# Kernel optimization log

Hardware: AMD Instinct MI355X
Metric: run time of the kernel (lower is better)

Reference implementation:

```python
import jax, jax.numpy as jnp
import numpy as np

B, L = 4096, 200
USER_COUNT, ITEM_COUNT, CATE_COUNT = 100000, 100000, 1000
USER_DIM, ITEM_DIM, CATE_DIM = 128, 64, 64
BN_EPS = 1e-5


def setup_inputs() -> dict:
    key = jax.random.key(0)
    ks = jax.random.split(key, 16)
    # ragged history: valid prefix of `length` items (ids >= 1), zero-padded tail
    length = jax.random.randint(ks[3], (B,), 1, L + 1)
    hist_raw = jax.random.randint(ks[2], (B, L), 1, ITEM_COUNT)
    history = jnp.where(jnp.arange(L)[None, :] < length[:, None], hist_raw, 0)
    inp = {
        "user": jax.random.randint(ks[0], (B,), 0, USER_COUNT),
        "item": jax.random.randint(ks[1], (B,), 0, ITEM_COUNT),
        "history": history,
        "length": length,
        "cate_list": jax.random.randint(ks[4], (ITEM_COUNT,), 0, CATE_COUNT),
        "user_emb_W": jax.random.normal(ks[5], (USER_COUNT, USER_DIM), jnp.float32) * 0.05,
        "item_emb_W": jax.random.normal(ks[6], (ITEM_COUNT, ITEM_DIM), jnp.float32) * 0.05,
        "cate_emb_W": jax.random.normal(ks[7], (CATE_COUNT, CATE_DIM), jnp.float32) * 0.05,
        "bn_gamma": 1.0 + 0.1 * jax.random.normal(ks[8], (384,), jnp.float32),
        "bn_beta": 0.1 * jax.random.normal(ks[9], (384,), jnp.float32),
        "W1": jax.random.normal(ks[10], (200, 384), jnp.float32) * (1.0 / np.sqrt(384)),
        "b1": jnp.zeros((200,), jnp.float32),
        "a1": jnp.full((), 0.25, jnp.float32),
        "W2": jax.random.normal(ks[11], (80, 200), jnp.float32) * (1.0 / np.sqrt(200)),
        "b2": jnp.zeros((80,), jnp.float32),
        "a2": jnp.full((), 0.25, jnp.float32),
        "W3": jax.random.normal(ks[12], (2, 80), jnp.float32) * (1.0 / np.sqrt(80)),
        "b3": jnp.zeros((2,), jnp.float32),
    }
    return inp


def _prelu(x, a):
    return jnp.where(x >= 0, x, a * x)


def reference(user, item, history, length, cate_list,
              user_emb_W, item_emb_W, cate_emb_W, bn_gamma, bn_beta,
              W1, b1, a1, W2, b2, a2, W3, b3):
    u = user_emb_W[user]                                              # [B,128]
    it = jnp.concatenate([item_emb_W[item], cate_emb_W[cate_list[item]]], -1)  # [B,128]

    # Faithful replication of get_emb's loop semantics:
    # row b uses the prefix of `history[b]` up to (and incl.) the position
    # just before the first zero; a row whose first entry is 0 halts the
    # outer loop, zeroing that row and all following rows.
    nz = history != 0                                                 # [B,L]
    prefix = jnp.concatenate(
        [jnp.ones((history.shape[0], 1), bool),
         jnp.cumprod(nz[:, 1:].astype(jnp.int32), axis=1).astype(bool)], axis=1)
    row_active = jnp.cumprod(nz[:, 0].astype(jnp.int32)).astype(bool)  # outer break
    mask = prefix & row_active[:, None]                               # [B,L]

    he = jnp.concatenate([item_emb_W[history], cate_emb_W[cate_list[history]]], -1)  # [B,L,128]
    cnt = jnp.maximum(mask.sum(-1), 1).astype(he.dtype)               # [B]
    pooled = (he * mask[..., None].astype(he.dtype)).sum(1) / cnt[:, None]  # [B,128]

    x = jnp.concatenate([u, it, pooled], -1)                          # [B,384]
    # BatchNorm1d in training mode (batch stats, biased variance)
    mean = x.mean(0)
    var = x.var(0)
    x = (x - mean) * jax.lax.rsqrt(var + BN_EPS) * bn_gamma + bn_beta
    x = _prelu(x @ W1.T + b1, a1)
    x = _prelu(x @ W2.T + b2, a2)
    x = x @ W3.T + b3
    return jax.nn.softmax(x, axis=1)
```

## Files before the change

kernel.cpp:

```cpp
#include <hip/hip_runtime.h>
#include <hip/hip_bf16.h>

#define B_SZ 4096
#define L_SZ 200
#define ITEM_ELEMS 6400000
#define CATE_ELEMS 64000

typedef __bf16 bf16x8 __attribute__((ext_vector_type(8)));
typedef float  f32x4  __attribute__((ext_vector_type(4)));

static __device__ inline unsigned short bfbits(float f) {
    return __builtin_bit_cast(unsigned short, (__bf16)f);
}
static __device__ inline float bf2f(unsigned short u) {
    return __builtin_bit_cast(float, (unsigned int)u << 16);
}

__global__ __launch_bounds__(256) void k_prep(
    const float* __restrict__ W1, const float* __restrict__ W2,
    ushort* __restrict__ W1f, ushort* __restrict__ W2f,
    const int* __restrict__ history, int* __restrict__ first_bad,
    float* __restrict__ acc,
    const float* __restrict__ item_W, const float* __restrict__ cate_W,
    ushort* __restrict__ item_bf, ushort* __restrict__ cate_bf)
{
    const int bid = blockIdx.x, tid = threadIdx.x;

    if (bid < 48) {
        const int lane = tid & 63, wv = tid >> 6;
        const int t = bid * 4 + wv;
        if (t >= 191) return;
        const int nr = lane & 15, quad = lane >> 4;
        ushort v[8];
        if (t < 156) {
            const int oT = t / 12, kS = t - oT * 12;
            const int o = oT * 16 + nr;
            #pragma unroll
            for (int j = 0; j < 8; ++j) {
                int k = kS * 32 + quad * 8 + j;
                v[j] = (o < 200) ? bfbits(W1[(size_t)o * 384 + k]) : (ushort)0;
            }
            ushort* dst = W1f + ((size_t)t * 64 + lane) * 8;
            *(ushort4*)(dst)     = make_ushort4(v[0], v[1], v[2], v[3]);
            *(ushort4*)(dst + 4) = make_ushort4(v[4], v[5], v[6], v[7]);
        } else {
            const int idx = t - 156;
            const int oT = idx / 7, kS = idx - oT * 7;
            const int o = oT * 16 + nr;
            #pragma unroll
            for (int j = 0; j < 8; ++j) {
                int k = kS * 32 + quad * 8 + j;
                v[j] = (k < 200) ? bfbits(W2[(size_t)o * 200 + k]) : (ushort)0;
            }
            ushort* dst = W2f + ((size_t)idx * 64 + lane) * 8;
            *(ushort4*)(dst)     = make_ushort4(v[0], v[1], v[2], v[3]);
            *(ushort4*)(dst + 4) = make_ushort4(v[4], v[5], v[6], v[7]);
        }
        return;
    }

    if (bid == 48) {
        acc[tid] = 0.f; acc[256 + tid] = 0.f; acc[512 + tid] = 0.f;
        int m = B_SZ;
        #pragma unroll
        for (int i = 0; i < 16; ++i) {
            int b = tid + i * 256;
            if (history[(size_t)b * L_SZ] == 0) m = min(m, b);
        }
        __shared__ int red[256];
        red[tid] = m;
        __syncthreads();
        for (int s = 128; s > 0; s >>= 1) {
            if (tid < s) red[tid] = min(red[tid], red[tid + s]);
            __syncthreads();
        }
        if (tid == 0) first_bad[0] = red[0];
        return;
    }

    if (bid == 49) {
        for (int i = tid * 8; i < CATE_ELEMS; i += 256 * 8) {
            float4 a = *(const float4*)(cate_W + i);
            float4 b = *(const float4*)(cate_W + i + 4);
            *(ushort4*)(cate_bf + i) =
                make_ushort4(bfbits(a.x), bfbits(a.y), bfbits(a.z), bfbits(a.w));
            *(ushort4*)(cate_bf + i + 4) =
                make_ushort4(bfbits(b.x), bfbits(b.y), bfbits(b.z), bfbits(b.w));
        }
        return;
    }

    {
        const size_t step = (size_t)(gridDim.x - 50) * 256 * 8;
        for (size_t i = ((size_t)(bid - 50) * 256 + tid) * 8; i < ITEM_ELEMS; i += step) {
            float4 a = *(const float4*)(item_W + i);
            float4 b = *(const float4*)(item_W + i + 4);
            *(ushort4*)(item_bf + i) =
                make_ushort4(bfbits(a.x), bfbits(a.y), bfbits(a.z), bfbits(a.w));
            *(ushort4*)(item_bf + i + 4) =
                make_ushort4(bfbits(b.x), bfbits(b.y), bfbits(b.z), bfbits(b.w));
        }
    }
}

__global__ __launch_bounds__(256) void k_pool(
    const int* __restrict__ user, const int* __restrict__ item,
    const int* __restrict__ history, const int* __restrict__ cate_list,
    const float* __restrict__ user_W, const ushort* __restrict__ item_bf,
    const ushort* __restrict__ cate_bf, const int* __restrict__ first_bad,
    ushort* __restrict__ xb)
{
    const int b = blockIdx.x;
    const int tid = threadIdx.x;
    __shared__ int sh_item[L_SZ];
    __shared__ int sh_cid[L_SZ];
    __shared__ int s_fz;
    __shared__ __align__(16) float red[8][128];
    if (tid == 0) s_fz = L_SZ;
    __syncthreads();
    if (tid < L_SZ) {
        int h = history[(size_t)b * L_SZ + tid];
        sh_item[tid] = h;
        if (tid >= 1 && h == 0) atomicMin(&s_fz, tid);
        sh_cid[tid] = cate_list[h];
    }
    __syncthreads();
    const bool active = (b < first_bad[0]);
    const int valid = active ? s_fz : 0;
    const float inv_cnt = 1.0f / (float)max(valid, 1);

    const int group = tid >> 5, lane = tid & 31;
    const int sub = lane >> 4, q = lane & 15;
    const ushort* tab = (sub == 0) ? item_bf : cate_bf;
    const int*    ids = (sub == 0) ? sh_item : sh_cid;
    float4 acc = make_float4(0.f, 0.f, 0.f, 0.f);
    int l = group;
    for (; l + 8 < valid; l += 16) {
        int id0 = ids[l], id1 = ids[l + 8];
        ushort4 v0 = ((const ushort4*)(tab + (size_t)id0 * 64))[q];
        ushort4 v1 = ((const ushort4*)(tab + (size_t)id1 * 64))[q];
        acc.x += bf2f(v0.x) + bf2f(v1.x);
        acc.y += bf2f(v0.y) + bf2f(v1.y);
        acc.z += bf2f(v0.z) + bf2f(v1.z);
        acc.w += bf2f(v0.w) + bf2f(v1.w);
    }
    if (l < valid) {
        int id = ids[l];
        ushort4 v = ((const ushort4*)(tab + (size_t)id * 64))[q];
        acc.x += bf2f(v.x); acc.y += bf2f(v.y);
        acc.z += bf2f(v.z); acc.w += bf2f(v.w);
    }
    *((float4*)&red[group][lane * 4]) = acc;
    __syncthreads();

    ushort* xrow = xb + (size_t)b * 384;
    if (tid < 128) {
        float s = 0.f;
        #pragma unroll
        for (int g = 0; g < 8; ++g) s += red[g][tid];
        xrow[256 + tid] = bfbits(s * inv_cnt);
        xrow[tid] = bfbits(user_W[(size_t)user[b] * 128 + tid]);
    } else if (tid < 192) {
        int f = tid - 128;
        xrow[128 + f] = item_bf[(size_t)item[b] * 64 + f];
    } else {
        int f = tid - 192;
        xrow[192 + f] = cate_bf[(size_t)cate_list[item[b]] * 64 + f];
    }
}

__global__ __launch_bounds__(384) void k_bnstats(const ushort* __restrict__ xb,
                                                 float* __restrict__ acc) {
    const int f = threadIdx.x;
    const int r0 = blockIdx.x * 16;
    float s = 0.f, s2 = 0.f;
    for (int r = r0; r < r0 + 16; ++r) {
        float v = bf2f(xb[(size_t)r * 384 + f]);
        s += v; s2 += v * v;
    }
    atomicAdd(&acc[f], s);
    atomicAdd(&acc[384 + f], s2);
}

__global__ __launch_bounds__(832) void k_l123(
    const ushort* __restrict__ xb, const float* __restrict__ accv,
    const float* __restrict__ gamma, const float* __restrict__ beta,
    const ushort* __restrict__ W1f, const float* __restrict__ b1,
    const float* __restrict__ a1p, const ushort* __restrict__ W2f,
    const float* __restrict__ b2, const float* __restrict__ a2p,
    const float* __restrict__ W3, const float* __restrict__ b3,
    float* __restrict__ out)
{
    __shared__ float As[384], Cs[384];
    __shared__ __align__(16) ushort h1s[16][232];
    const int tid = threadIdx.x;
    if (tid < 384) {
        const float inv_b = 1.0f / (float)B_SZ;
        float mean = accv[tid] * inv_b;
        float var  = accv[384 + tid] * inv_b - mean * mean;
        float a = gamma[tid] * rsqrtf(var + 1e-5f);
        As[tid] = a;
        Cs[tid] = beta[tid] - mean * a;
    }
    __syncthreads();

    const int lane = tid & 63, wv = tid >> 6;
    const int nr = lane & 15, quad = lane >> 4;
    const int mT = blockIdx.x;
    const int oT = wv;
    const int o = oT * 16 + nr;
    const float a1 = a1p[0];

    float bias = (o < 200) ? b1[o] : 0.f;
    f32x4 acc = {bias, bias, bias, bias};
    const ushort* xrow = xb + (size_t)(mT * 16 + nr) * 384;

    for (int kS = 0; kS < 12; ++kS) {
        const int kc = kS * 32 + quad * 8;
        bf16x8 a8 = *(const bf16x8*)(xrow + kc);
        float4 A0 = *(const float4*)&As[kc],     A1 = *(const float4*)&As[kc + 4];
        float4 C0 = *(const float4*)&Cs[kc],     C1 = *(const float4*)&Cs[kc + 4];
        bf16x8 w;
        w[0] = (__bf16)((float)a8[0] * A0.x + C0.x);
        w[1] = (__bf16)((float)a8[1] * A0.y + C0.y);
        w[2] = (__bf16)((float)a8[2] * A0.z + C0.z);
        w[3] = (__bf16)((float)a8[3] * A0.w + C0.w);
        w[4] = (__bf16)((float)a8[4] * A1.x + C1.x);
        w[5] = (__bf16)((float)a8[5] * A1.y + C1.y);
        w[6] = (__bf16)((float)a8[6] * A1.z + C1.z);
        w[7] = (__bf16)((float)a8[7] * A1.w + C1.w);
        bf16x8 bfr = *(const bf16x8*)(W1f + (((size_t)oT * 12 + kS) * 64 + lane) * 8);
        acc = __builtin_amdgcn_mfma_f32_16x16x32_bf16(w, bfr, acc, 0, 0, 0);
    }

    #pragma unroll
    for (int r = 0; r < 4; ++r) {
        int row = quad * 4 + r;
        float s = acc[r];
        s = (s >= 0.f) ? s : a1 * s;
        h1s[row][o] = bfbits(s);
        if (oT == 12) h1s[row][o + 16] = 0;
    }
    __syncthreads();

    if (wv != 0) return;

    const float a2 = a2p[0];
    f32x4 acc2[5];
    #pragma unroll
    for (int i = 0; i < 5; ++i) {
        float bb = b2[i * 16 + nr];
        acc2[i] = (f32x4){bb, bb, bb, bb};
    }
    for (int kS = 0; kS < 7; ++kS) {
        bf16x8 a8 = *(const bf16x8*)(&h1s[nr][kS * 32 + quad * 8]);
        #pragma unroll
        for (int i = 0; i < 5; ++i) {
            bf16x8 bfr = *(const bf16x8*)(W2f + (((size_t)i * 7 + kS) * 64 + lane) * 8);
            acc2[i] = __builtin_amdgcn_mfma_f32_16x16x32_bf16(a8, bfr, acc2[i], 0, 0, 0);
        }
    }

    float w0[5], w1[5];
    #pragma unroll
    for (int i = 0; i < 5; ++i) {
        w0[i] = W3[i * 16 + nr];
        w1[i] = W3[80 + i * 16 + nr];
    }
    f32x4 p0 = {0.f, 0.f, 0.f, 0.f}, p1 = {0.f, 0.f, 0.f, 0.f};
    #pragma unroll
    for (int i = 0; i < 5; ++i) {
        #pragma unroll
        for (int r = 0; r < 4; ++r) {
            float s = acc2[i][r];
            s = (s >= 0.f) ? s : a2 * s;
            p0[r] += s * w0[i];
            p1[r] += s * w1[i];
        }
    }
    #pragma unroll
    for (int m = 1; m < 16; m <<= 1) {
        #pragma unroll
        for (int r = 0; r < 4; ++r) {
            p0[r] += __shfl_xor(p0[r], m, 64);
            p1[r] += __shfl_xor(p1[r], m, 64);
        }
    }
    if (nr == 0) {
        float B0 = b3[0], B1 = b3[1];
        #pragma unroll
        for (int r = 0; r < 4; ++r) {
            float l0 = p0[r] + B0, l1 = p1[r] + B1;
            float mx = fmaxf(l0, l1);
            float e0 = expf(l0 - mx), e1 = expf(l1 - mx);
            float inv = 1.0f / (e0 + e1);
            int row = mT * 16 + quad * 4 + r;
            *(float2*)(out + (size_t)row * 2) = make_float2(e0 * inv, e1 * inv);
        }
    }
}

extern "C" void kernel_launch(void* const* d_in, const int* in_sizes, int n_in,
                              void* d_out, int out_size, void* d_ws, size_t ws_size,
                              hipStream_t stream) {
    const int*   user      = (const int*)  d_in[0];
    const int*   item      = (const int*)  d_in[1];
    const int*   history   = (const int*)  d_in[2];
    const int*   cate_list = (const int*)  d_in[4];
    const float* user_W    = (const float*)d_in[5];
    const float* item_W    = (const float*)d_in[6];
    const float* cate_W    = (const float*)d_in[7];
    const float* gamma     = (const float*)d_in[8];
    const float* beta      = (const float*)d_in[9];
    const float* W1        = (const float*)d_in[10];
    const float* b1        = (const float*)d_in[11];
    const float* a1        = (const float*)d_in[12];
    const float* W2        = (const float*)d_in[13];
    const float* b2        = (const float*)d_in[14];
    const float* a2        = (const float*)d_in[15];
    const float* W3        = (const float*)d_in[16];
    const float* b3        = (const float*)d_in[17];
    float* out = (float*)d_out;

    char* ws = (char*)d_ws;
    int*    first_bad = (int*)   ws;
    float*  acc       = (float*)(ws + 64);
    ushort* xb        = (ushort*)(ws + 3200);
    ushort* W1f       = (ushort*)(ws + 3148928);
    ushort* W2f       = (ushort*)(ws + 3308672);
    ushort* cate_bf   = (ushort*)(ws + 3344512);
    ushort* item_bf   = (ushort*)(ws + 3472512);

    hipLaunchKernelGGL(k_prep,    dim3(1074), dim3(256), 0, stream,
                       W1, W2, W1f, W2f, history, first_bad, acc,
                       item_W, cate_W, item_bf, cate_bf);
    hipLaunchKernelGGL(k_pool,    dim3(B_SZ), dim3(256), 0, stream,
                       user, item, history, cate_list, user_W, item_bf, cate_bf,
                       first_bad, xb);
    hipLaunchKernelGGL(k_bnstats, dim3(256),  dim3(384), 0, stream, xb, acc);
    hipLaunchKernelGGL(k_l123,    dim3(256),  dim3(832), 0, stream,
                       xb, acc, gamma, beta, W1f, b1, a1, W2f, b2, a2, W3, b3, out);
}
```

Baseline: 179.4 us.

## Gather fp32 embeddings directly and fuse BN statistics into pooling kernel

Stops converting the whole item and category embedding tables to bf16 on every call. The pooling kernel now gathers fp32 rows directly, which removes a full read and write pass over the roughly 25 MB item table, at the price of twice the bytes per gathered row. The separate BN-stats kernel is also removed: the pooling kernel atomically accumulates per-feature sum and sum-of-squares into 16 slot copies, and the MLP kernel reduces those slots. This drops a launch and a re-read of xb, but adds heavy atomic traffic with contention on 16 copies of each address.

```diff
diff --git a/kernel.cpp b/kernel.cpp
--- a/kernel.cpp
+++ b/kernel.cpp
@@ -3,8 +3,6 @@
 
 #define B_SZ 4096
 #define L_SZ 200
-#define ITEM_ELEMS 6400000
-#define CATE_ELEMS 64000
 
 typedef __bf16 bf16x8 __attribute__((ext_vector_type(8)));
 typedef float  f32x4  __attribute__((ext_vector_type(4)));
@@ -20,9 +18,7 @@
     const float* __restrict__ W1, const float* __restrict__ W2,
     ushort* __restrict__ W1f, ushort* __restrict__ W2f,
     const int* __restrict__ history, int* __restrict__ first_bad,
-    float* __restrict__ acc,
-    const float* __restrict__ item_W, const float* __restrict__ cate_W,
-    ushort* __restrict__ item_bf, ushort* __restrict__ cate_bf)
+    float* __restrict__ acc)
 {
     const int bid = blockIdx.x, tid = threadIdx.x;
 
@@ -59,56 +55,29 @@
         return;
     }
 
-    if (bid == 48) {
-        acc[tid] = 0.f; acc[256 + tid] = 0.f; acc[512 + tid] = 0.f;
-        int m = B_SZ;
-        #pragma unroll
-        for (int i = 0; i < 16; ++i) {
-            int b = tid + i * 256;
-            if (history[(size_t)b * L_SZ] == 0) m = min(m, b);
-        }
-        __shared__ int red[256];
-        red[tid] = m;
+    for (int i = tid; i < 16 * 768; i += 256) acc[i] = 0.f;
+    int m = B_SZ;
+    #pragma unroll
+    for (int i = 0; i < 16; ++i) {
+        int b = tid + i * 256;
+        if (history[(size_t)b * L_SZ] == 0) m = min(m, b);
+    }
+    __shared__ int red[256];
+    red[tid] = m;
+    __syncthreads();
+    for (int s = 128; s > 0; s >>= 1) {
+        if (tid < s) red[tid] = min(red[tid], red[tid + s]);
         __syncthreads();
-        for (int s = 128; s > 0; s >>= 1) {
-            if (tid < s) red[tid] = min(red[tid], red[tid + s]);
-            __syncthreads();
-        }
-        if (tid == 0) first_bad[0] = red[0];
-        return;
-    }
-
-    if (bid == 49) {
-        for (int i = tid * 8; i < CATE_ELEMS; i += 256 * 8) {
-            float4 a = *(const float4*)(cate_W + i);
-            float4 b = *(const float4*)(cate_W + i + 4);
-            *(ushort4*)(cate_bf + i) =
-                make_ushort4(bfbits(a.x), bfbits(a.y), bfbits(a.z), bfbits(a.w));
-            *(ushort4*)(cate_bf + i + 4) =
-                make_ushort4(bfbits(b.x), bfbits(b.y), bfbits(b.z), bfbits(b.w));
-        }
-        return;
-    }
-
-    {
-        const size_t step = (size_t)(gridDim.x - 50) * 256 * 8;
-        for (size_t i = ((size_t)(bid - 50) * 256 + tid) * 8; i < ITEM_ELEMS; i += step) {
-            float4 a = *(const float4*)(item_W + i);
-            float4 b = *(const float4*)(item_W + i + 4);
-            *(ushort4*)(item_bf + i) =
-                make_ushort4(bfbits(a.x), bfbits(a.y), bfbits(a.z), bfbits(a.w));
-            *(ushort4*)(item_bf + i + 4) =
-                make_ushort4(bfbits(b.x), bfbits(b.y), bfbits(b.z), bfbits(b.w));
-        }
-    }
+    }
+    if (tid == 0) first_bad[0] = red[0];
 }
 
 __global__ __launch_bounds__(256) void k_pool(
     const int* __restrict__ user, const int* __restrict__ item,
     const int* __restrict__ history, const int* __restrict__ cate_list,
-    const float* __restrict__ user_W, const ushort* __restrict__ item_bf,
-    const ushort* __restrict__ cate_bf, const int* __restrict__ first_bad,
-    ushort* __restrict__ xb)
+    const float* __restrict__ user_W, const float* __restrict__ item_W,
+    const float* __restrict__ cate_W, const int* __restrict__ first_bad,
+    ushort* __restrict__ xb, float* __restrict__ acc_slots)
 {
     const int b = blockIdx.x;
     const int tid = threadIdx.x;
@@ -131,55 +100,50 @@
 
     const int group = tid >> 5, lane = tid & 31;
     const int sub = lane >> 4, q = lane & 15;
-    const ushort* tab = (sub == 0) ? item_bf : cate_bf;
-    const int*    ids = (sub == 0) ? sh_item : sh_cid;
+    const float* tab = (sub == 0) ? item_W : cate_W;
+    const int*   ids = (sub == 0) ? sh_item : sh_cid;
     float4 acc = make_float4(0.f, 0.f, 0.f, 0.f);
     int l = group;
     for (; l + 8 < valid; l += 16) {
         int id0 = ids[l], id1 = ids[l + 8];
-        ushort4 v0 = ((const ushort4*)(tab + (size_t)id0 * 64))[q];
-        ushort4 v1 = ((const ushort4*)(tab + (size_t)id1 * 64))[q];
-        acc.x += bf2f(v0.x) + bf2f(v1.x);
-        acc.y += bf2f(v0.y) + bf2f(v1.y);
-        acc.z += bf2f(v0.z) + bf2f(v1.z);
-        acc.w += bf2f(v0.w) + bf2f(v1.w);
+        float4 v0 = ((const float4*)(tab + (size_t)id0 * 64))[q];
+        float4 v1 = ((const float4*)(tab + (size_t)id1 * 64))[q];
+        acc.x += v0.x + v1.x; acc.y += v0.y + v1.y;
+        acc.z += v0.z + v1.z; acc.w += v0.w + v1.w;
     }
     if (l < valid) {
         int id = ids[l];
-        ushort4 v = ((const ushort4*)(tab + (size_t)id * 64))[q];
-        acc.x += bf2f(v.x); acc.y += bf2f(v.y);
-        acc.z += bf2f(v.z); acc.w += bf2f(v.w);
+        float4 v = ((const float4*)(tab + (size_t)id * 64))[q];
+        acc.x += v.x; acc.y += v.y; acc.z += v.z; acc.w += v.w;
     }
     *((float4*)&red[group][lane * 4]) = acc;
     __syncthreads();
 
+    float* accs = acc_slots + (size_t)(b & 15) * 768;
     ushort* xrow = xb + (size_t)b * 384;
     if (tid < 128) {
         float s = 0.f;
         #pragma unroll
         for (int g = 0; g < 8; ++g) s += red[g][tid];
-        xrow[256 + tid] = bfbits(s * inv_cnt);
-        xrow[tid] = bfbits(user_W[(size_t)user[b] * 128 + tid]);
+        float pv = s * inv_cnt;
+        xrow[256 + tid] = bfbits(pv);
+        atomicAdd(&accs[256 + tid], pv);
+        atomicAdd(&accs[640 + tid], pv * pv);
+        float uv = user_W[(size_t)user[b] * 128 + tid];
+        xrow[tid] = bfbits(uv);
+        atomicAdd(&accs[tid], uv);
+        atomicAdd(&accs[384 + tid], uv * uv);
     } else if (tid < 192) {
-        int f = tid - 128;
-        xrow[128 + f] = item_bf[(size_t)item[b] * 64 + f];
+        float v = item_W[(size_t)item[b] * 64 + (tid - 128)];
+        xrow[tid] = bfbits(v);
+        atomicAdd(&accs[tid], v);
+        atomicAdd(&accs[384 + tid], v * v);
     } else {
-        int f = tid - 192;
-        xrow[192 + f] = cate_bf[(size_t)cate_list[item[b]] * 64 + f];
-    }
-}
-
-__global__ __launch_bounds__(384) void k_bnstats(const ushort* __restrict__ xb,
-                                                 float* __restrict__ acc) {
-    const int f = threadIdx.x;
-    const int r0 = blockIdx.x * 16;
-    float s = 0.f, s2 = 0.f;
-    for (int r = r0; r < r0 + 16; ++r) {
-        float v = bf2f(xb[(size_t)r * 384 + f]);
-        s += v; s2 += v * v;
-    }
-    atomicAdd(&acc[f], s);
-    atomicAdd(&acc[384 + f], s2);
+        float v = cate_W[(size_t)cate_list[item[b]] * 64 + (tid - 192)];
+        xrow[tid] = bfbits(v);
+        atomicAdd(&accs[tid], v);
+        atomicAdd(&accs[384 + tid], v * v);
+    }
 }
 
 __global__ __launch_bounds__(832) void k_l123(
@@ -195,9 +159,15 @@
     __shared__ __align__(16) ushort h1s[16][232];
     const int tid = threadIdx.x;
     if (tid < 384) {
+        float s = 0.f, s2 = 0.f;
+        #pragma unroll
+        for (int sl = 0; sl < 16; ++sl) {
+            s  += accv[sl * 768 + tid];
+            s2 += accv[sl * 768 + 384 + tid];
+        }
         const float inv_b = 1.0f / (float)B_SZ;
-        float mean = accv[tid] * inv_b;
-        float var  = accv[384 + tid] * inv_b - mean * mean;
+        float mean = s * inv_b;
+        float var  = s2 * inv_b - mean * mean;
         float a = gamma[tid] * rsqrtf(var + 1e-5f);
         As[tid] = a;
         Cs[tid] = beta[tid] - mean * a;
@@ -325,19 +295,15 @@
     char* ws = (char*)d_ws;
     int*    first_bad = (int*)   ws;
     float*  acc       = (float*)(ws + 64);
-    ushort* xb        = (ushort*)(ws + 3200);
-    ushort* W1f       = (ushort*)(ws + 3148928);
-    ushort* W2f       = (ushort*)(ws + 3308672);
-    ushort* cate_bf   = (ushort*)(ws + 3344512);
-    ushort* item_bf   = (ushort*)(ws + 3472512);
-
-    hipLaunchKernelGGL(k_prep,    dim3(1074), dim3(256), 0, stream,
-                       W1, W2, W1f, W2f, history, first_bad, acc,
-                       item_W, cate_W, item_bf, cate_bf);
-    hipLaunchKernelGGL(k_pool,    dim3(B_SZ), dim3(256), 0, stream,
-                       user, item, history, cate_list, user_W, item_bf, cate_bf,
-                       first_bad, xb);
-    hipLaunchKernelGGL(k_bnstats, dim3(256),  dim3(384), 0, stream, xb, acc);
-    hipLaunchKernelGGL(k_l123,    dim3(256),  dim3(832), 0, stream,
+    ushort* xb        = (ushort*)(ws + 49216);
+    ushort* W1f       = (ushort*)(ws + 3194944);
+    ushort* W2f       = (ushort*)(ws + 3354688);
+
+    hipLaunchKernelGGL(k_prep, dim3(49),   dim3(256), 0, stream,
+                       W1, W2, W1f, W2f, history, first_bad, acc);
+    hipLaunchKernelGGL(k_pool, dim3(B_SZ), dim3(256), 0, stream,
+                       user, item, history, cate_list, user_W, item_W, cate_W,
+                       first_bad, xb, acc);
+    hipLaunchKernelGGL(k_l123, dim3(256),  dim3(832), 0, stream,
                        xb, acc, gamma, beta, W1f, b1, a1, W2f, b2, a2, W3, b3, out);
 }
```

New measurement: 173.8 us. 1.03x faster.
